# Performance work log

Measured on AMD Instinct MI355X. Metric: run time of the kernel, lower is better.

Reference implementation:

```python
import jax, jax.numpy as jnp
import numpy as np

B, T, C = 4, 2048, 1024
H = 16
D = C // H  # 64


def setup_inputs() -> dict:
    key = jax.random.key(0)
    ks = jax.random.split(key, 5)
    scale = 0.02
    x = jax.random.normal(ks[0], (B, T, C), dtype=jnp.float32)
    # Linear weights stored in [in, out] layout (equivalent to torch W.T)
    W_qkv = jax.random.normal(ks[1], (C, 3 * C), dtype=jnp.float32) * scale
    b_qkv = jax.random.normal(ks[2], (3 * C,), dtype=jnp.float32) * scale
    W_out = jax.random.normal(ks[3], (C, C), dtype=jnp.float32) * scale
    b_out = jax.random.normal(ks[4], (C,), dtype=jnp.float32) * scale
    return {"x": x, "W_qkv": W_qkv, "b_qkv": b_qkv, "W_out": W_out, "b_out": b_out}


def reference(x, W_qkv, b_qkv, W_out, b_out):
    Bx, Tx, Cx = x.shape
    qkv = x @ W_qkv + b_qkv                      # [B,T,3C]
    qkv = qkv.reshape(Bx, Tx, 3, H, D)
    q = jnp.transpose(qkv[:, :, 0], (0, 2, 1, 3))  # [B,H,T,D]
    k = jnp.transpose(qkv[:, :, 1], (0, 2, 1, 3))
    v = jnp.transpose(qkv[:, :, 2], (0, 2, 1, 3))
    scores = jnp.einsum('bhqd,bhkd->bhqk', q, k) / jnp.sqrt(jnp.float32(D))
    causal = jnp.tril(jnp.ones((Tx, Tx), dtype=bool))  # keep lower triangle
    scores = jnp.where(causal, scores, jnp.float32(-jnp.inf))
    w = jax.nn.softmax(scores, axis=-1)           # dropout p=0.0 (eval)
    out = jnp.einsum('bhqk,bhkd->bhqd', w, v)     # [B,H,T,D]
    out = jnp.transpose(out, (0, 2, 1, 3)).reshape(Bx, Tx, Cx)
    return out @ W_out + b_out
```

## Files before the change

kernel.cpp:

```cpp
#include <hip/hip_runtime.h>

typedef _Float16 f16;
typedef _Float16 f16x4 __attribute__((ext_vector_type(4)));
typedef _Float16 f16x8 __attribute__((ext_vector_type(8)));
typedef float    f32x4 __attribute__((ext_vector_type(4)));

#define B_ 4
#define T_ 2048
#define C_ 1024
#define H_ 16
#define D_ 64

#if __has_builtin(__builtin_amdgcn_exp2f)
#define FAST_EXP(x) __builtin_amdgcn_exp2f(x)
#define QSCALE (0.125f * 1.44269504f)
#define POFF 8.0f
#else
#define FAST_EXP(x) __expf(x)
#define QSCALE 0.125f
#define POFF 5.5452f
#endif

__device__ __forceinline__ void gload_lds16(const f16* g, f16* l) {
  __builtin_amdgcn_global_load_lds(
      (const __attribute__((address_space(1))) unsigned int*)g,
      (__attribute__((address_space(3))) unsigned int*)l, 16, 0, 0);
}

__global__ void cvt_kernel(const float* __restrict__ in, f16* __restrict__ out, int n4) {
  int i = blockIdx.x * blockDim.x + threadIdx.x;
  int stride = gridDim.x * blockDim.x;
  for (; i < n4; i += stride) {
    float4 v = ((const float4*)in)[i];
    f16x4 h = { (f16)v.x, (f16)v.y, (f16)v.z, (f16)v.w };
    ((f16x4*)out)[i] = h;
  }
}

__global__ void transpose2_kernel(const float* __restrict__ Wqkv, f16* __restrict__ WqkvT,
                                  const float* __restrict__ Wout, f16* __restrict__ WoutT) {
  __shared__ f16 tile[32][33];
  const int K = 1024;
  int bx = blockIdx.x, by = blockIdx.y;
  const float* W; f16* Wt; int N;
  if (bx < 96) { W = Wqkv; Wt = WqkvT; N = 3072; }
  else         { W = Wout; Wt = WoutT; N = 1024; bx -= 96; }
  int tx = threadIdx.x & 31, ty = threadIdx.x >> 5;
  #pragma unroll
  for (int i = ty; i < 32; i += 8)
    tile[i][tx] = (f16)W[(size_t)(by * 32 + i) * N + bx * 32 + tx];
  __syncthreads();
  #pragma unroll
  for (int i = ty; i < 32; i += 8)
    Wt[(size_t)(bx * 32 + i) * K + by * 32 + tx] = tile[tx][i];
}

template <int EPI>
__global__ __launch_bounds__(256, 3)
void gemm_kernel(const f16* __restrict__ A, const f16* __restrict__ Bt,
                 const float* __restrict__ bias, float* __restrict__ outF,
                 f16* __restrict__ q, f16* __restrict__ kk, f16* __restrict__ vt,
                 int M, int N, int K) {
  __shared__ __align__(16) f16 As[3][128 * 32];
  __shared__ __align__(16) f16 Bs[3][128 * 32];
  const int nbn = N >> 7;
  const int bid = blockIdx.x;
  const int bm = bid / nbn, bn = bid % nbn;
  const int m0 = bm << 7, n0 = bn << 7;
  const int tid = threadIdx.x;
  const int lane = tid & 63, wid = tid >> 6;
  const int wr = wid >> 1, wc = wid & 1;

  f32x4 acc[4][4] = {};

  const int srow = lane >> 2;
  const int scol = (((lane & 3) ^ ((lane >> 3) & 3)) << 3);
  const f16* Abase = A + (size_t)(m0 + srow) * K + scol;
  const f16* Bbase = Bt + (size_t)(n0 + srow) * K + scol;

  auto stage = [&](int buf, int kt) {
    const int c0 = wid * 2;
    #pragma unroll
    for (int c = c0; c < c0 + 2; ++c) {
      gload_lds16(Abase + (size_t)c * 16 * K + kt * 32, &As[buf][c * 512]);
      gload_lds16(Bbase + (size_t)c * 16 * K + kt * 32, &Bs[buf][c * 512]);
    }
  };

  const int g = lane >> 4;
  const int rr = lane & 15;
  const int swz = (g ^ ((rr >> 1) & 3)) << 4;

  auto compute = [&](int buf) {
    f16x8 af[4], bf[4];
    #pragma unroll
    for (int t = 0; t < 4; ++t) {
      af[t] = *(const f16x8*)((const char*)&As[buf][0] + (wr * 64 + t * 16 + rr) * 64 + swz);
      bf[t] = *(const f16x8*)((const char*)&Bs[buf][0] + (wc * 64 + t * 16 + rr) * 64 + swz);
    }
    __builtin_amdgcn_s_setprio(1);
    #pragma unroll
    for (int i = 0; i < 4; ++i)
      #pragma unroll
      for (int j = 0; j < 4; ++j)
        acc[i][j] = __builtin_amdgcn_mfma_f32_16x16x32_f16(af[i], bf[j], acc[i][j], 0, 0, 0);
    __builtin_amdgcn_s_setprio(0);
  };

  const int nk = K >> 5;
  int bcur = 0, bnext = 1, bnn = 2;
  stage(0, 0);
  stage(1, 1);
  asm volatile("s_waitcnt vmcnt(4)" ::: "memory");
  __builtin_amdgcn_s_barrier();
  __builtin_amdgcn_sched_barrier(0);
  for (int t = 0; t < nk; ++t) {
    if (t + 2 < nk) stage(bnn, t + 2);
    compute(bcur);
    if (t + 1 < nk) {
      if (t + 2 < nk) asm volatile("s_waitcnt vmcnt(4)" ::: "memory");
      else            asm volatile("s_waitcnt vmcnt(0)" ::: "memory");
      __builtin_amdgcn_s_barrier();
      __builtin_amdgcn_sched_barrier(0);
    }
    const int tmp = bcur; bcur = bnext; bnext = bnn; bnn = tmp;
  }

  const int col = lane & 15;
  const int row4 = (lane >> 4) << 2;
  #pragma unroll
  for (int i = 0; i < 4; ++i) {
    #pragma unroll
    for (int j = 0; j < 4; ++j) {
      const int n = n0 + wc * 64 + j * 16 + col;
      const float bn_ = bias[n];
      #pragma unroll
      for (int r = 0; r < 4; ++r) {
        const int m = m0 + wr * 64 + i * 16 + row4 + r;
        const float v = acc[i][j][r] + bn_;
        if (EPI == 1) {
          outF[(size_t)m * N + n] = v;
        } else {
          const int which = n >> 10;
          const int cc = n & 1023;
          const int h = cc >> 6, d = cc & 63;
          const int b = m >> 11, t = m & 2047;
          const size_t bh = (size_t)b * 16 + h;
          const f16 hv = (f16)v;
          if (which == 0)      q [(bh * T_ + t) * D_ + d] = hv;
          else if (which == 1) kk[(bh * T_ + t) * D_ + d] = hv;
          else                 vt[(bh * D_ + d) * T_ + t] = hv;
        }
      }
    }
  }
}

__global__ __launch_bounds__(256, 3)
void attn_kernel(const f16* __restrict__ Q, const f16* __restrict__ Kg,
                 const f16* __restrict__ Vt, f16* __restrict__ Aout) {
  __shared__ __align__(16) f16 Ks[2][64 * 64];
  __shared__ __align__(16) f16 Vs[2][64 * 64];
  __shared__ __align__(16) f16 Pt[4][32 * 64];

  const int bid = blockIdx.x;
  const int xcd = bid & 7, k = bid >> 3;
  const int bh = (xcd << 3) + (k & 7);
  const int ti = 15 - (k >> 3);
  const int lane = threadIdx.x & 63, w = threadIdx.x >> 6;
  const int col = lane & 15;
  const int g = lane >> 4;
  const int ko = g << 3;

  const f16* Qp = Q + (size_t)bh * T_ * D_;
  const f16* Kp = Kg + (size_t)bh * T_ * D_;
  const f16* Vp = Vt + (size_t)bh * D_ * T_;

  const int sr = lane >> 3;
  const int sc = ((lane & 7) ^ (sr & 7)) << 3;

  auto stage = [&](int buf, int kb) {
    #pragma unroll
    for (int c2 = 0; c2 < 2; ++c2) {
      const int c = (w << 1) + c2;
      gload_lds16(Kp + (size_t)(kb + (c << 3) + sr) * D_ + sc, &Ks[buf][c * 512]);
      gload_lds16(Vp + (size_t)((c << 3) + sr) * T_ + kb + sc, &Vs[buf][c * 512]);
    }
  };
  auto ldsK = [&](int buf, int krow, int d0) -> f16x8 {
    const int off = krow * 128 + ((d0 << 1) ^ ((krow & 7) << 4));
    return *(const f16x8*)((const char*)&Ks[buf][0] + off);
  };
  auto ldsV = [&](int buf, int drow, int k0) -> f16x8 {
    const int off = drow * 128 + ((k0 << 1) ^ ((drow & 7) << 4));
    return *(const f16x8*)((const char*)&Vs[buf][0] + off);
  };

  char* PtW = (char*)&Pt[w][0];
  const int b = bh >> 4, hd = bh & 15;

  const int qrow0 = (ti << 7) + (w << 5);
  const int nkt = (ti << 1) + 2;

  const f16 qsc = (f16)QSCALE;
  f16x8 qf[2][2];
  #pragma unroll
  for (int h = 0; h < 2; ++h)
    #pragma unroll
    for (int s = 0; s < 2; ++s) {
      f16x8 t = *(const f16x8*)&Qp[(size_t)(qrow0 + h * 16 + col) * D_ + s * 32 + ko];
      #pragma unroll
      for (int e = 0; e < 8; ++e) t[e] = t[e] * qsc;
      qf[h][s] = t;
    }

  f32x4 o[2][4] = {};
  f32x4 lpv[2] = {};

  auto COMPUTE = [&](int buf, int kb) {
    f32x4 sc2[2][4] = {};
    __builtin_amdgcn_s_setprio(1);
    #pragma unroll
    for (int s = 0; s < 2; ++s)
      #pragma unroll
      for (int mt = 0; mt < 4; ++mt) {
        f16x8 kf = ldsK(buf, mt * 16 + col, s * 32 + ko);
        sc2[0][mt] = __builtin_amdgcn_mfma_f32_16x16x32_f16(kf, qf[0][s], sc2[0][mt], 0, 0, 0);
        sc2[1][mt] = __builtin_amdgcn_mfma_f32_16x16x32_f16(kf, qf[1][s], sc2[1][mt], 0, 0, 0);
      }
    __builtin_amdgcn_s_setprio(0);

    if (kb + 63 > qrow0) {
      #pragma unroll
      for (int mt = 0; mt < 4; ++mt)
        #pragma unroll
        for (int r = 0; r < 4; ++r) {
          const int kv = kb + mt * 16 + (g << 2) + r;
          if (kv > qrow0 + col)      sc2[0][mt][r] = -1e30f;
          if (kv > qrow0 + 16 + col) sc2[1][mt][r] = -1e30f;
        }
    }

    #pragma unroll
    for (int h = 0; h < 2; ++h) {
      #pragma unroll
      for (int mt = 0; mt < 4; ++mt) {
        f16x4 ph;
        #pragma unroll
        for (int r = 0; r < 4; ++r) {
          const float p = FAST_EXP(sc2[h][mt][r] - POFF);
          lpv[h][r] += p;
          ph[r] = (f16)p;
        }
        *(f16x4*)(PtW + (h * 16 + col) * 128 + (((mt << 5) + (g << 3)) ^ ((col & 7) << 4))) = ph;
      }
    }

    __builtin_amdgcn_s_setprio(1);
    #pragma unroll
    for (int s = 0; s < 2; ++s) {
      const int pcb = ((s << 6) + (g << 4)) ^ ((col & 7) << 4);
      f16x8 pb0 = *(const f16x8*)(PtW + col * 128 + pcb);
      f16x8 pb1 = *(const f16x8*)(PtW + (16 + col) * 128 + pcb);
      #pragma unroll
      for (int mt = 0; mt < 4; ++mt) {
        f16x8 vf = ldsV(buf, mt * 16 + col, s * 32 + ko);
        o[0][mt] = __builtin_amdgcn_mfma_f32_16x16x32_f16(vf, pb0, o[0][mt], 0, 0, 0);
        o[1][mt] = __builtin_amdgcn_mfma_f32_16x16x32_f16(vf, pb1, o[1][mt], 0, 0, 0);
      }
    }
    __builtin_amdgcn_s_setprio(0);
  };

  stage(0, 0);
  asm volatile("s_waitcnt vmcnt(0)" ::: "memory");
  __builtin_amdgcn_s_barrier();
  __builtin_amdgcn_sched_barrier(0);

  #pragma unroll 1
  for (int kt = 0; kt < nkt; ++kt) {
    if (kt + 1 < nkt) stage((kt + 1) & 1, (kt + 1) << 6);
    if ((kt << 6) <= qrow0 + 31) COMPUTE(kt & 1, kt << 6);

    __builtin_amdgcn_sched_barrier(0);
    asm volatile("s_waitcnt vmcnt(0)" ::: "memory");
    __builtin_amdgcn_s_barrier();
    __builtin_amdgcn_sched_barrier(0);
  }

  #pragma unroll
  for (int h = 0; h < 2; ++h) {
    float l = lpv[h][0] + lpv[h][1] + lpv[h][2] + lpv[h][3];
    l += __shfl_xor(l, 16, 64);
    l += __shfl_xor(l, 32, 64);
    const float inv = 1.0f / l;
    const int t = qrow0 + h * 16 + col;
    const size_t rowoff = ((size_t)b * T_ + t) * C_ + (size_t)hd * D_;
    #pragma unroll
    for (int mt = 0; mt < 4; ++mt) {
      f16x4 ov;
      #pragma unroll
      for (int r = 0; r < 4; ++r) ov[r] = (f16)(o[h][mt][r] * inv);
      *(f16x4*)&Aout[rowoff + mt * 16 + (g << 2)] = ov;
    }
  }
}

extern "C" void kernel_launch(void* const* d_in, const int* in_sizes, int n_in,
                              void* d_out, int out_size, void* d_ws, size_t ws_size,
                              hipStream_t stream) {
  const float* x    = (const float*)d_in[0];
  const float* Wqkv = (const float*)d_in[1];
  const float* bqkv = (const float*)d_in[2];
  const float* Wout = (const float*)d_in[3];
  const float* bout = (const float*)d_in[4];
  float* out = (float*)d_out;

  char* ws = (char*)d_ws;
  f16* xb     = (f16*)ws;
  f16* Wqkv_t = (f16*)(ws + (16u << 20));
  f16* Wout_t = (f16*)(ws + (22u << 20));
  f16* Qb     = (f16*)(ws + (24u << 20));
  f16* Kb     = (f16*)(ws + (40u << 20));
  f16* Vtb    = (f16*)(ws + (56u << 20));

  cvt_kernel<<<2048, 256, 0, stream>>>(x, xb, (B_ * T_ * C_) / 4);
  dim3 gt(128, 32);
  transpose2_kernel<<<gt, 256, 0, stream>>>(Wqkv, Wqkv_t, Wout, Wout_t);

  gemm_kernel<0><<<64 * 24, 256, 0, stream>>>(xb, Wqkv_t, bqkv, nullptr,
                                              Qb, Kb, Vtb, 8192, 3072, 1024);
  attn_kernel<<<1024, 256, 0, stream>>>(Qb, Kb, Vtb, xb );
  gemm_kernel<1><<<64 * 8, 256, 0, stream>>>(xb, Wout_t, bout, out,
                                             nullptr, nullptr, nullptr, 8192, 1024, 1024);
}
```

Measured before the change: 189.4 us.

## Enlarge GEMM tiles to 128x256 with 512 threads, BK=64 and XCD-aware block mapping

The shared GEMM kernel now uses 512-thread workgroups computing 128x256 output tiles with a 64-wide K step, three-stage LDS buffering and an 8-column XOR swizzle. Block IDs are remapped so consecutive tiles land on the same XCD, which is meant to improve L2 reuse. The larger tile raises arithmetic intensity per global load and halves the number of barriers per K. In exchange it uses much more LDS (about 144KB) and only one workgroup per CU, which lowers occupancy and gives fewer blocks for the output projection (256 blocks).

```diff
diff --git a/kernel.cpp b/kernel.cpp
--- a/kernel.cpp
+++ b/kernel.cpp
@@ -56,47 +56,52 @@
 }
 
 template <int EPI>
-__global__ __launch_bounds__(256, 3)
+__global__ __launch_bounds__(512, 1)
 void gemm_kernel(const f16* __restrict__ A, const f16* __restrict__ Bt,
                  const float* __restrict__ bias, float* __restrict__ outF,
-                 f16* __restrict__ q, f16* __restrict__ kk, f16* __restrict__ vt,
+                 f16* __restrict__ q, f16* __restrict__ kk2, f16* __restrict__ vt,
                  int M, int N, int K) {
-  __shared__ __align__(16) f16 As[3][128 * 32];
-  __shared__ __align__(16) f16 Bs[3][128 * 32];
-  const int nbn = N >> 7;
+  __shared__ __align__(16) f16 As[3][128 * 64];
+  __shared__ __align__(16) f16 Bs[3][256 * 64];
+  const int nbn = N >> 8;
   const int bid = blockIdx.x;
-  const int bm = bid / nbn, bn = bid % nbn;
-  const int m0 = bm << 7, n0 = bn << 7;
+  const int nwg = (M >> 7) * nbn;
+  const int cpx = nwg >> 3;
+  const int wg = (bid & 7) * cpx + (bid >> 3);
+  const int bm = wg / nbn, bn = wg % nbn;
+  const int m0 = bm << 7, n0 = bn << 8;
   const int tid = threadIdx.x;
   const int lane = tid & 63, wid = tid >> 6;
-  const int wr = wid >> 1, wc = wid & 1;
+  const int wm = wid >> 2, wnn = wid & 3;
 
   f32x4 acc[4][4] = {};
 
-  const int srow = lane >> 2;
-  const int scol = (((lane & 3) ^ ((lane >> 3) & 3)) << 3);
+  const int srow = (wid << 3) + (lane >> 3);
+  const int scol = (((lane & 7) ^ ((lane >> 3) & 7)) << 3);
   const f16* Abase = A + (size_t)(m0 + srow) * K + scol;
   const f16* Bbase = Bt + (size_t)(n0 + srow) * K + scol;
 
-  auto stage = [&](int buf, int kt) {
-    const int c0 = wid * 2;
-    #pragma unroll
-    for (int c = c0; c < c0 + 2; ++c) {
-      gload_lds16(Abase + (size_t)c * 16 * K + kt * 32, &As[buf][c * 512]);
-      gload_lds16(Bbase + (size_t)c * 16 * K + kt * 32, &Bs[buf][c * 512]);
-    }
+  auto stage = [&](int slot, int t) {
+    const f16* as = Abase + (size_t)t * 64;
+    const f16* bs = Bbase + (size_t)t * 64;
+    gload_lds16(as,                    &As[slot][wid * 512]);
+    gload_lds16(as + (size_t)64 * K,   &As[slot][wid * 512 + 4096]);
+    #pragma unroll
+    for (int j = 0; j < 4; ++j)
+      gload_lds16(bs + (size_t)j * 64 * K, &Bs[slot][wid * 512 + j * 4096]);
   };
 
   const int g = lane >> 4;
   const int rr = lane & 15;
-  const int swz = (g ^ ((rr >> 1) & 3)) << 4;
-
-  auto compute = [&](int buf) {
+  const int rsw = (rr & 7) << 4;
+
+  auto compute = [&](int slot, int kk) {
+    const int cb = ((kk << 6) + (g << 4)) ^ rsw;
     f16x8 af[4], bf[4];
     #pragma unroll
     for (int t = 0; t < 4; ++t) {
-      af[t] = *(const f16x8*)((const char*)&As[buf][0] + (wr * 64 + t * 16 + rr) * 64 + swz);
-      bf[t] = *(const f16x8*)((const char*)&Bs[buf][0] + (wc * 64 + t * 16 + rr) * 64 + swz);
+      af[t] = *(const f16x8*)((const char*)&As[slot][0] + (wm * 64 + t * 16 + rr) * 128 + cb);
+      bf[t] = *(const f16x8*)((const char*)&Bs[slot][0] + (wnn * 64 + t * 16 + rr) * 128 + cb);
     }
     __builtin_amdgcn_s_setprio(1);
     #pragma unroll
@@ -107,23 +112,24 @@
     __builtin_amdgcn_s_setprio(0);
   };
 
-  const int nk = K >> 5;
-  int bcur = 0, bnext = 1, bnn = 2;
+  const int NT = K >> 6;
   stage(0, 0);
   stage(1, 1);
-  asm volatile("s_waitcnt vmcnt(4)" ::: "memory");
+  asm volatile("s_waitcnt vmcnt(6)" ::: "memory");
   __builtin_amdgcn_s_barrier();
   __builtin_amdgcn_sched_barrier(0);
-  for (int t = 0; t < nk; ++t) {
-    if (t + 2 < nk) stage(bnn, t + 2);
-    compute(bcur);
-    if (t + 1 < nk) {
-      if (t + 2 < nk) asm volatile("s_waitcnt vmcnt(4)" ::: "memory");
-      else            asm volatile("s_waitcnt vmcnt(0)" ::: "memory");
-      __builtin_amdgcn_s_barrier();
-      __builtin_amdgcn_sched_barrier(0);
-    }
-    const int tmp = bcur; bcur = bnext; bnext = bnn; bnn = tmp;
+
+  int s0 = 0, s1 = 1, s2 = 2;
+  #pragma unroll 1
+  for (int t = 0; t < NT; ++t) {
+    if (t + 2 < NT) stage(s2, t + 2);
+    compute(s0, 0);
+    compute(s0, 1);
+    if (t + 2 < NT) asm volatile("s_waitcnt vmcnt(6)" ::: "memory");
+    else            asm volatile("s_waitcnt vmcnt(0)" ::: "memory");
+    __builtin_amdgcn_s_barrier();
+    __builtin_amdgcn_sched_barrier(0);
+    const int tmp = s0; s0 = s1; s1 = s2; s2 = tmp;
   }
 
   const int col = lane & 15;
@@ -132,11 +138,11 @@
   for (int i = 0; i < 4; ++i) {
     #pragma unroll
     for (int j = 0; j < 4; ++j) {
-      const int n = n0 + wc * 64 + j * 16 + col;
+      const int n = n0 + wnn * 64 + j * 16 + col;
       const float bn_ = bias[n];
       #pragma unroll
       for (int r = 0; r < 4; ++r) {
-        const int m = m0 + wr * 64 + i * 16 + row4 + r;
+        const int m = m0 + wm * 64 + i * 16 + row4 + r;
         const float v = acc[i][j][r] + bn_;
         if (EPI == 1) {
           outF[(size_t)m * N + n] = v;
@@ -144,12 +150,12 @@
           const int which = n >> 10;
           const int cc = n & 1023;
           const int h = cc >> 6, d = cc & 63;
-          const int b = m >> 11, t = m & 2047;
+          const int b = m >> 11, tt = m & 2047;
           const size_t bh = (size_t)b * 16 + h;
           const f16 hv = (f16)v;
-          if (which == 0)      q [(bh * T_ + t) * D_ + d] = hv;
-          else if (which == 1) kk[(bh * T_ + t) * D_ + d] = hv;
-          else                 vt[(bh * D_ + d) * T_ + t] = hv;
+          if (which == 0)      q  [(bh * T_ + tt) * D_ + d] = hv;
+          else if (which == 1) kk2[(bh * T_ + tt) * D_ + d] = hv;
+          else                 vt [(bh * D_ + d) * T_ + tt] = hv;
         }
       }
     }
@@ -328,9 +334,9 @@
   dim3 gt(128, 32);
   transpose2_kernel<<<gt, 256, 0, stream>>>(Wqkv, Wqkv_t, Wout, Wout_t);
 
-  gemm_kernel<0><<<64 * 24, 256, 0, stream>>>(xb, Wqkv_t, bqkv, nullptr,
-                                              Qb, Kb, Vtb, 8192, 3072, 1024);
+  gemm_kernel<0><<<768, 512, 0, stream>>>(xb, Wqkv_t, bqkv, nullptr,
+                                          Qb, Kb, Vtb, 8192, 3072, 1024);
   attn_kernel<<<1024, 256, 0, stream>>>(Qb, Kb, Vtb, xb );
-  gemm_kernel<1><<<64 * 8, 256, 0, stream>>>(xb, Wout_t, bout, out,
-                                             nullptr, nullptr, nullptr, 8192, 1024, 1024);
-}
+  gemm_kernel<1><<<256, 512, 0, stream>>>(xb, Wout_t, bout, out,
+                                          nullptr, nullptr, nullptr, 8192, 1024, 1024);
+}
```

Result: slower. 199.3 us (+5.3%).
